# Kernel tuning notes

Hardware: AMD Instinct MI355X
Metric: run time of the kernel (lower is better)

The kernel has to match this reference:

```python
import jax, jax.numpy as jnp
import numpy as np

N_NODES = 50000
NEG_SLOPE = 0.2


def gat_conv(x, src, dst, W, att_src, att_dst, bias, concat):
    # x: [N, F_in], W: [H*D, F_in], att_*: [H, D], bias: [H*D] or [D]
    N = x.shape[0]
    H, D = att_src.shape
    h = (x @ W.T).reshape(N, H, D)                      # [N, H, D]
    a_src = jnp.einsum('nhd,hd->nh', h, att_src)        # [N, H]
    a_dst = jnp.einsum('nhd,hd->nh', h, att_dst)        # [N, H]
    e = jax.nn.leaky_relu(a_src[src] + a_dst[dst], NEG_SLOPE)  # [E, H]
    # softmax over incoming edges of each destination node
    m = jax.ops.segment_max(e, dst, num_segments=N)     # [N, H]
    ex = jnp.exp(e - m[dst])
    denom = jax.ops.segment_sum(ex, dst, num_segments=N)
    alpha = ex / denom[dst]                             # [E, H]
    msg = alpha[:, :, None] * h[src]                    # [E, H, D]
    out = jax.ops.segment_sum(msg, dst, num_segments=N) # [N, H, D]
    out = out.reshape(N, H * D) if concat else out.mean(axis=1)
    return out + bias


def setup_inputs() -> dict:
    key = jax.random.key(0)
    ks = jax.random.split(key, 10)
    nfeat, nhid, nclass, heads = 256, 128, 40, 4
    d1 = nhid // heads  # 32
    E = 800000
    x = jax.random.normal(ks[0], (N_NODES, nfeat), dtype=jnp.float32)
    edge_index = jax.random.randint(ks[1], (2, E), 0, N_NODES, dtype=jnp.int64)
    s = 0.1
    W1 = jax.random.normal(ks[2], (heads * d1, nfeat), dtype=jnp.float32) * s
    att_src1 = jax.random.normal(ks[3], (heads, d1), dtype=jnp.float32) * s
    att_dst1 = jax.random.normal(ks[4], (heads, d1), dtype=jnp.float32) * s
    b1 = jnp.zeros((heads * d1,), dtype=jnp.float32)
    W2 = jax.random.normal(ks[5], (nclass, nhid), dtype=jnp.float32) * s
    att_src2 = jax.random.normal(ks[6], (1, nclass), dtype=jnp.float32) * s
    att_dst2 = jax.random.normal(ks[7], (1, nclass), dtype=jnp.float32) * s
    b2 = jnp.zeros((nclass,), dtype=jnp.float32)
    return {"x": x, "edge_index": edge_index, "W1": W1, "att_src1": att_src1,
            "att_dst1": att_dst1, "b1": b1, "W2": W2, "att_src2": att_src2,
            "att_dst2": att_dst2, "b2": b2}


def reference(x, edge_index, W1, att_src1, att_dst1, b1, W2, att_src2, att_dst2, b2):
    # PyG GATConv adds self-loops by default
    loops = jnp.arange(N_NODES, dtype=edge_index.dtype)
    src = jnp.concatenate([edge_index[0], loops])
    dst = jnp.concatenate([edge_index[1], loops])
    h = gat_conv(x, src, dst, W1, att_src1, att_dst1, b1, concat=True)
    h = jax.nn.relu(h)
    # dropout is identity in eval mode
    out = gat_conv(h, src, dst, W2, att_src2, att_dst2, b2, concat=True)
    return out
```

## Files before the change

kernel.cpp:

```cpp
#include <hip/hip_runtime.h>
#include <hip/hip_bf16.h>
#include <cstdint>
#include <cstddef>

#define N_NODES 50000
#define NEG_SLOPE 0.2f
#define NB 196
#define BIN_CHUNK 8192
#define SLICE_MAX 14336

typedef float floatx4 __attribute__((ext_vector_type(4)));
typedef short shortx8 __attribute__((ext_vector_type(8)));

__device__ __forceinline__ unsigned short f2b(float f) {
    union { float f; unsigned u; } v; v.f = f;
    unsigned u = v.u;
    return (unsigned short)((u + 0x7FFFu + ((u >> 16) & 1u)) >> 16);
}
__device__ __forceinline__ float b2f(unsigned short b) {
    union { unsigned u; float f; } v; v.u = ((unsigned)b) << 16;
    return v.f;
}

__global__ __launch_bounds__(256) void bucket_hist_kernel(
    const int* __restrict__ ei, int E0, int E, int* __restrict__ bhist) {
    __shared__ int h[NB];
    int t = threadIdx.x;
    for (int i = t; i < NB; i += 256) h[i] = 0;
    __syncthreads();
    int base = blockIdx.x * BIN_CHUNK;
    int end = min(base + BIN_CHUNK, E);
    for (int e = base + t; e < end; e += 256) {
        int d = (e < E0) ? ei[E0 + e] : (e - E0);
        atomicAdd(&h[d >> 8], 1);
    }
    __syncthreads();
    for (int i = t; i < NB; i += 256)
        if (h[i]) atomicAdd(&bhist[i], h[i]);
}

__global__ __launch_bounds__(256) void bucket_scan_kernel(
    const int* __restrict__ bhist, int* __restrict__ bbase,
    int* __restrict__ bcursor, int* __restrict__ rowptr, int E) {
    __shared__ int buf[256];
    int t = threadIdx.x;
    int v = (t < NB) ? bhist[t] : 0;
    int x = v;
    for (int off = 1; off < 256; off <<= 1) {
        buf[t] = x; __syncthreads();
        int y = (t >= off) ? buf[t - off] : 0;
        __syncthreads();
        x += y;
    }
    if (t < NB) {
        bbase[t] = x - v;
        bcursor[t] = x - v;
    }
    if (t == NB - 1) bbase[NB] = x;
    if (t == 0) rowptr[N_NODES] = E;
}

__global__ __launch_bounds__(256) void bin_kernel(
    const int* __restrict__ ei, int E0, int E,
    int* __restrict__ bcursor, unsigned int* __restrict__ ebuf) {
    __shared__ int h[NB];
    __shared__ int gbase[NB];
    int t = threadIdx.x;
    for (int i = t; i < NB; i += 256) h[i] = 0;
    __syncthreads();
    int base = blockIdx.x * BIN_CHUNK;
    int end = min(base + BIN_CHUNK, E);
    for (int e = base + t; e < end; e += 256) {
        int d = (e < E0) ? ei[E0 + e] : (e - E0);
        atomicAdd(&h[d >> 8], 1);
    }
    __syncthreads();
    for (int i = t; i < NB; i += 256) {
        int c = h[i];
        gbase[i] = c ? atomicAdd(&bcursor[i], c) : 0;
        h[i] = 0;
    }
    __syncthreads();
    for (int e = base + t; e < end; e += 256) {
        int s, d;
        if (e < E0) { s = ei[e]; d = ei[E0 + e]; }
        else        { s = e - E0; d = e - E0; }
        int b = d >> 8;
        int off = atomicAdd(&h[b], 1);
        ebuf[gbase[b] + off] = (unsigned)s | ((unsigned)(d & 255) << 16);
    }
}

__global__ __launch_bounds__(256) void build_kernel(
    const unsigned int* __restrict__ ebuf, const int* __restrict__ bbase,
    int* __restrict__ rowptr, int* __restrict__ csr_src) {
    __shared__ int h[256];
    __shared__ int lrp[257];
    __shared__ int stag[SLICE_MAX];
    int b = blockIdx.x, t = threadIdx.x;
    int e0 = bbase[b], e1 = bbase[b + 1];
    int cnt = e1 - e0;
    int n0 = b << 8;
    h[t] = 0;
    __syncthreads();
    for (int i = t; i < cnt; i += 256)
        atomicAdd(&h[ebuf[e0 + i] >> 16], 1);
    __syncthreads();
    int v = h[t], x = v;
    __shared__ int buf[256];
    for (int off = 1; off < 256; off <<= 1) {
        buf[t] = x; __syncthreads();
        int y = (t >= off) ? buf[t - off] : 0;
        __syncthreads();
        x += y;
    }
    lrp[t] = x - v;
    if (t == 255) lrp[256] = x;
    h[t] = 0;
    __syncthreads();
    int n = n0 + t;
    if (n < N_NODES) rowptr[n] = e0 + lrp[t];
    for (int i = t; i < cnt; i += 256) {
        unsigned int v2 = ebuf[e0 + i];
        int dloc = v2 >> 16;
        int off = atomicAdd(&h[dloc], 1);
        stag[lrp[dloc] + off] = (int)(v2 & 0xFFFFu);
    }
    __syncthreads();
    for (int i = t; i < cnt; i += 256) csr_src[e0 + i] = stag[i];
}

template <int BM, int BN, int NREAL, int KK, typename InT>
__global__ __launch_bounds__(256) void gemm_bf16_kernel(
    const InT* __restrict__ A, const float* __restrict__ B,
    unsigned short* __restrict__ Cb, int M) {
    const int BK = 64, LDK = 72;
    const int NT = BN / 16;
    __shared__ unsigned short As[BM * LDK];
    __shared__ unsigned short Bs[BN * LDK];
    const int t = threadIdx.x;
    const int wave = t >> 6, lane = t & 63;
    const int lrow = lane & 15, lkg = lane >> 4;
    const int bm = blockIdx.x * BM;

    floatx4 acc[NT] = {};

    for (int k0 = 0; k0 < KK; k0 += BK) {
        __syncthreads();
        if constexpr (sizeof(InT) == 4) {
            for (int i = t; i < BM * 16; i += 256) {
                int r = i >> 4, c4 = (i & 15) << 2;
                int gr = bm + r;
                float4 v = make_float4(0.f, 0.f, 0.f, 0.f);
                if (gr < M) v = *(const float4*)&A[(size_t)gr * KK + k0 + c4];
                int o = r * LDK + c4;
                As[o] = f2b(v.x); As[o + 1] = f2b(v.y);
                As[o + 2] = f2b(v.z); As[o + 3] = f2b(v.w);
            }
        } else {
            for (int i = t; i < BM * 8; i += 256) {
                int r = i >> 3, c8 = (i & 7) << 3;
                int gr = bm + r;
                shortx8 v = {};
                if (gr < M) v = *(const shortx8*)&A[(size_t)gr * KK + k0 + c8];
                *(shortx8*)&As[r * LDK + c8] = v;
            }
        }
        for (int i = t; i < BN * 16; i += 256) {
            int r = i >> 4, c4 = (i & 15) << 2;
            float4 v = make_float4(0.f, 0.f, 0.f, 0.f);
            if (r < NREAL) v = *(const float4*)&B[(size_t)r * KK + k0 + c4];
            int o = r * LDK + c4;
            Bs[o] = f2b(v.x); Bs[o + 1] = f2b(v.y);
            Bs[o + 2] = f2b(v.z); Bs[o + 3] = f2b(v.w);
        }
        __syncthreads();

        for (int ks = 0; ks < BK; ks += 32) {
            int kc = ks + lkg * 8;
            int row = wave * 16 + lrow;
            shortx8 a = *(const shortx8*)&As[row * LDK + kc];
#pragma unroll
            for (int nt = 0; nt < NT; nt++) {
                shortx8 b = *(const shortx8*)&Bs[(nt * 16 + lrow) * LDK + kc];
                acc[nt] = __builtin_amdgcn_mfma_f32_16x16x32_bf16(a, b, acc[nt], 0, 0, 0);
            }
        }
    }
#pragma unroll
    for (int nt = 0; nt < NT; nt++)
#pragma unroll
        for (int r = 0; r < 4; r++) {
            int row = bm + wave * 16 + lkg * 4 + r;
            int col = nt * 16 + lrow;
            if (row < M && col < NREAL)
                Cb[(size_t)row * NREAL + col] = f2b(acc[nt][r]);
        }
}

__global__ void att1_kernel(const unsigned short* __restrict__ h1b,
                            const float* __restrict__ att_src,
                            const float* __restrict__ att_dst,
                            float* __restrict__ a_src, float* __restrict__ a_dst,
                            int N) {
    int i = blockIdx.x * blockDim.x + threadIdx.x;
    if (i >= N * 4) return;
    int h = i & 3;
    const ushort4* hp = (const ushort4*)(h1b + (size_t)i * 32);
    const float4* as = (const float4*)(att_src + h * 32);
    const float4* ad = (const float4*)(att_dst + h * 32);
    float ssum = 0.f, dsum = 0.f;
#pragma unroll
    for (int j = 0; j < 8; j++) {
        ushort4 hv = hp[j];
        float4 av = as[j], dv = ad[j];
        float x0 = b2f(hv.x), x1 = b2f(hv.y), x2 = b2f(hv.z), x3 = b2f(hv.w);
        ssum += x0 * av.x + x1 * av.y + x2 * av.z + x3 * av.w;
        dsum += x0 * dv.x + x1 * dv.y + x2 * dv.z + x3 * dv.w;
    }
    a_src[i] = ssum;
    a_dst[i] = dsum;
}

__global__ void att2_kernel(const unsigned short* __restrict__ h2b,
                            const float* __restrict__ att_src,
                            const float* __restrict__ att_dst,
                            float* __restrict__ a_src, float* __restrict__ a_dst,
                            int N) {
    int n = blockIdx.x * blockDim.x + threadIdx.x;
    if (n >= N) return;
    const ushort4* hp = (const ushort4*)(h2b + (size_t)n * 40);
    const float4* as = (const float4*)att_src;
    const float4* ad = (const float4*)att_dst;
    float ssum = 0.f, dsum = 0.f;
#pragma unroll
    for (int j = 0; j < 10; j++) {
        ushort4 hv = hp[j];
        float4 av = as[j], dv = ad[j];
        float x0 = b2f(hv.x), x1 = b2f(hv.y), x2 = b2f(hv.z), x3 = b2f(hv.w);
        ssum += x0 * av.x + x1 * av.y + x2 * av.z + x3 * av.w;
        dsum += x0 * dv.x + x1 * dv.y + x2 * dv.z + x3 * dv.w;
    }
    a_src[n] = ssum;
    a_dst[n] = dsum;
}

__global__ __launch_bounds__(256) void agg1_kernel(
    const unsigned short* __restrict__ h1b, const float* __restrict__ a_src,
    const float* __restrict__ a_dst, const int* __restrict__ rowptr,
    const int* __restrict__ csr_src, const float* __restrict__ b1,
    unsigned short* __restrict__ zb, int N) {
    int wave = threadIdx.x >> 6, lane = threadIdx.x & 63;
    int n = blockIdx.x * 4 + wave;
    if (n >= N) return;
    int eg = lane >> 4;
    int fpos = lane & 15;
    int hd = fpos >> 2;
    int lidx = lane >> 2;
    int lh = lane & 3;
    float adn = a_dst[n * 4 + lh];
    int beg = rowptr[n], deg = rowptr[n + 1] - beg;

    float acc[8] = {0.f, 0.f, 0.f, 0.f, 0.f, 0.f, 0.f, 0.f};
    float den = 0.f;

    int s_e = (lidx < deg) ? csr_src[beg + lidx] : 0;
    float asv = a_src[(s_e << 2) + lh];

    for (int c0 = 0; c0 < deg; c0 += 16) {
        float l = asv + adn;
        l = l > 0.f ? l : NEG_SLOPE * l;
        float w_e = (c0 + lidx < deg) ? __expf(l) : 0.f;
        int cnt = min(16, deg - c0);
        int s4[4]; float w4[4]; shortx8 v4[4];
#pragma unroll
        for (int q = 0; q < 4; q++) {
            int el = (q << 2) + eg;
            s4[q] = __shfl(s_e, el << 2);
            w4[q] = __shfl(w_e, (el << 2) + hd);
        }
#pragma unroll
        for (int q = 0; q < 4; q++) {
            if (q * 4 < cnt)
                v4[q] = *(const shortx8*)&h1b[(size_t)s4[q] * 128 + fpos * 8];
        }
        int nidx = c0 + 16 + lidx;
        int s_n = (nidx < deg) ? csr_src[beg + nidx] : 0;
        float asn = a_src[(s_n << 2) + lh];
#pragma unroll
        for (int q = 0; q < 4; q++) {
            if (q * 4 < cnt) {
                float w = w4[q];
                den += w;
#pragma unroll
                for (int j = 0; j < 8; j++)
                    acc[j] += w * b2f((unsigned short)v4[q][j]);
            }
        }
        s_e = s_n; asv = asn;
    }
#pragma unroll
    for (int j = 0; j < 8; j++) {
        acc[j] += __shfl_xor(acc[j], 16);
        acc[j] += __shfl_xor(acc[j], 32);
    }
    den += __shfl_xor(den, 16);
    den += __shfl_xor(den, 32);
    if (lane < 16) {
        float inv = 1.f / den;
        float4 bb0 = *(const float4*)&b1[fpos * 8];
        float4 bb1 = *(const float4*)&b1[fpos * 8 + 4];
        shortx8 r;
        r[0] = (short)f2b(fmaxf(acc[0] * inv + bb0.x, 0.f));
        r[1] = (short)f2b(fmaxf(acc[1] * inv + bb0.y, 0.f));
        r[2] = (short)f2b(fmaxf(acc[2] * inv + bb0.z, 0.f));
        r[3] = (short)f2b(fmaxf(acc[3] * inv + bb0.w, 0.f));
        r[4] = (short)f2b(fmaxf(acc[4] * inv + bb1.x, 0.f));
        r[5] = (short)f2b(fmaxf(acc[5] * inv + bb1.y, 0.f));
        r[6] = (short)f2b(fmaxf(acc[6] * inv + bb1.z, 0.f));
        r[7] = (short)f2b(fmaxf(acc[7] * inv + bb1.w, 0.f));
        *(shortx8*)&zb[(size_t)n * 128 + fpos * 8] = r;
    }
}

__global__ __launch_bounds__(256) void agg2_kernel(
    const unsigned short* __restrict__ h2b, const float* __restrict__ a_src,
    const float* __restrict__ a_dst, const int* __restrict__ rowptr,
    const int* __restrict__ csr_src, const float* __restrict__ b2,
    float* __restrict__ out, int N) {
    int wave = threadIdx.x >> 6, lane = threadIdx.x & 63;
    int n = blockIdx.x * 4 + wave;
    if (n >= N) return;
    int eg = (lane >= 40) ? 2 : (lane >= 20 ? 1 : 0);
    int fp = lane - eg * 20;
    bool act = fp < 20;
    float adn = a_dst[n];
    int beg = rowptr[n], deg = rowptr[n + 1] - beg;

    float2 acc = {0.f, 0.f};
    float den = 0.f;
    for (int c0 = 0; c0 < deg; c0 += 48) {
        int idx = c0 + lane;
        bool cv = (lane < 48) && (idx < deg);
        int s_e = cv ? csr_src[beg + idx] : 0;
        float l = a_src[s_e] + adn;
        l = l > 0.f ? l : NEG_SLOPE * l;
        float w_e = cv ? __expf(l) : 0.f;
        int cnt = min(48, deg - c0);
#pragma unroll
        for (int qq = 0; qq < 4; qq++) {
            if (qq * 12 < cnt) {
                int s4[4]; float w4[4]; ushort2 v4[4];
#pragma unroll
                for (int q = 0; q < 4; q++) {
                    int el = qq * 12 + q * 3 + eg;
                    s4[q] = __shfl(s_e, el);
                    w4[q] = __shfl(w_e, el);
                }
#pragma unroll
                for (int q = 0; q < 4; q++) {
                    if (act)
                        v4[q] = *(const ushort2*)&h2b[(size_t)s4[q] * 40 + fp * 2];
                }
#pragma unroll
                for (int q = 0; q < 4; q++) {
                    float w = w4[q];
                    den += w;
                    if (act) {
                        acc.x += w * b2f(v4[q].x);
                        acc.y += w * b2f(v4[q].y);
                    }
                }
            }
        }
    }
    float a1x = __shfl(acc.x, fp + 20), a2x = __shfl(acc.x, fp + 40);
    float a1y = __shfl(acc.y, fp + 20), a2y = __shfl(acc.y, fp + 40);
    float d1  = __shfl(den,  fp + 20), d2  = __shfl(den,  fp + 40);
    if (lane < 20) {
        float sx = acc.x + a1x + a2x;
        float sy = acc.y + a1y + a2y;
        float dtot = den + d1 + d2;
        float inv = 1.f / dtot;
        float2 bb = *(const float2*)&b2[fp * 2];
        float2 o;
        o.x = sx * inv + bb.x;
        o.y = sy * inv + bb.y;
        *(float2*)&out[(size_t)n * 40 + fp * 2] = o;
    }
}

extern "C" void kernel_launch(void* const* d_in, const int* in_sizes, int n_in,
                              void* d_out, int out_size, void* d_ws, size_t ws_size,
                              hipStream_t stream) {
    const float* x        = (const float*)d_in[0];
    const int*   ei       = (const int*)d_in[1];
    const float* W1       = (const float*)d_in[2];
    const float* att_src1 = (const float*)d_in[3];
    const float* att_dst1 = (const float*)d_in[4];
    const float* b1       = (const float*)d_in[5];
    const float* W2       = (const float*)d_in[6];
    const float* att_src2 = (const float*)d_in[7];
    const float* att_dst2 = (const float*)d_in[8];
    const float* b2       = (const float*)d_in[9];
    float* out = (float*)d_out;

    const int N  = N_NODES;
    const int E0 = in_sizes[1] / 2;
    const int E  = E0 + N;
    const int NBLK = (E + BIN_CHUNK - 1) / BIN_CHUNK;

    char* ws = (char*)d_ws;
    unsigned short* h1b = (unsigned short*)(ws + 0);
    unsigned short* zb  = (unsigned short*)(ws + 12800000);
    unsigned short* h2b = (unsigned short*)(ws + 25600000);
    float* a_src1 = (float*)(ws + 29600000);
    float* a_dst1 = (float*)(ws + 30400000);
    float* a_src2 = (float*)(ws + 31200000);
    float* a_dst2 = (float*)(ws + 31400000);
    int*   rowptr = (int*)(ws + 31600000);
    int*   bhist  = (int*)(ws + 31800192);
    int*   bbase  = (int*)(ws + 31801088);
    int*   bcursor= (int*)(ws + 31801984);
    unsigned int* ebuf = (unsigned int*)(ws + 31802880);
    int*   csr_src= (int*)(ws + 35202880);

    hipMemsetAsync(bhist, 0, NB * sizeof(int), stream);

    bucket_hist_kernel<<<NBLK, 256, 0, stream>>>(ei, E0, E, bhist);
    bucket_scan_kernel<<<1, 256, 0, stream>>>(bhist, bbase, bcursor, rowptr, E);
    bin_kernel<<<NBLK, 256, 0, stream>>>(ei, E0, E, bcursor, ebuf);
    build_kernel<<<NB, 256, 0, stream>>>(ebuf, bbase, rowptr, csr_src);

    gemm_bf16_kernel<64, 128, 128, 256, float>
        <<<(N + 63) / 64, 256, 0, stream>>>(x, W1, h1b, N);
    att1_kernel<<<(N * 4 + 255) / 256, 256, 0, stream>>>(h1b, att_src1, att_dst1, a_src1, a_dst1, N);
    agg1_kernel<<<(N + 3) / 4, 256, 0, stream>>>(h1b, a_src1, a_dst1, rowptr, csr_src, b1, zb, N);

    gemm_bf16_kernel<64, 48, 40, 128, unsigned short>
        <<<(N + 63) / 64, 256, 0, stream>>>(zb, W2, h2b, N);
    att2_kernel<<<(N + 255) / 256, 256, 0, stream>>>(h2b, att_src2, att_dst2, a_src2, a_dst2, N);
    agg2_kernel<<<(N + 3) / 4, 256, 0, stream>>>(h2b, a_src2, a_dst2, rowptr, csr_src, b2, out, N);
}
```

Before: 243.3 us.

## Fuse attention dot products into GEMM epilogue and reuse per-block histograms in binning

The GEMM kernels now stage the bf16 output tile in shared memory, write it out with vectorized stores, and compute the per-node a_src/a_dst attention dot products in the same epilogue. This removes the separate att1/att2 kernels and their re-read of h. The first GEMM switches to a 128-row tile with two M sub-tiles per wave. Separately, the histogram kernel saves per-block bucket counts so the binning kernel can skip its second histogram pass over the destination indices, at the cost of an extra small workspace buffer.

Result: faster. 236.9 us (-2.7%).

```diff
diff --git a/kernel.cpp b/kernel.cpp
--- a/kernel.cpp
+++ b/kernel.cpp
@@ -23,7 +23,8 @@
 }
 
 __global__ __launch_bounds__(256) void bucket_hist_kernel(
-    const int* __restrict__ ei, int E0, int E, int* __restrict__ bhist) {
+    const int* __restrict__ ei, int E0, int E, int* __restrict__ bhist,
+    int* __restrict__ bhist_blk) {
     __shared__ int h[NB];
     int t = threadIdx.x;
     for (int i = t; i < NB; i += 256) h[i] = 0;
@@ -35,8 +36,11 @@
         atomicAdd(&h[d >> 8], 1);
     }
     __syncthreads();
-    for (int i = t; i < NB; i += 256)
-        if (h[i]) atomicAdd(&bhist[i], h[i]);
+    for (int i = t; i < NB; i += 256) {
+        int c = h[i];
+        bhist_blk[blockIdx.x * NB + i] = c;
+        if (c) atomicAdd(&bhist[i], c);
+    }
 }
 
 __global__ __launch_bounds__(256) void bucket_scan_kernel(
@@ -62,25 +66,19 @@
 
 __global__ __launch_bounds__(256) void bin_kernel(
     const int* __restrict__ ei, int E0, int E,
-    int* __restrict__ bcursor, unsigned int* __restrict__ ebuf) {
+    int* __restrict__ bcursor, unsigned int* __restrict__ ebuf,
+    const int* __restrict__ bhist_blk) {
     __shared__ int h[NB];
     __shared__ int gbase[NB];
     int t = threadIdx.x;
-    for (int i = t; i < NB; i += 256) h[i] = 0;
+    for (int i = t; i < NB; i += 256) {
+        int c = bhist_blk[blockIdx.x * NB + i];
+        gbase[i] = c ? atomicAdd(&bcursor[i], c) : 0;
+        h[i] = 0;
+    }
     __syncthreads();
     int base = blockIdx.x * BIN_CHUNK;
     int end = min(base + BIN_CHUNK, E);
-    for (int e = base + t; e < end; e += 256) {
-        int d = (e < E0) ? ei[E0 + e] : (e - E0);
-        atomicAdd(&h[d >> 8], 1);
-    }
-    __syncthreads();
-    for (int i = t; i < NB; i += 256) {
-        int c = h[i];
-        gbase[i] = c ? atomicAdd(&bcursor[i], c) : 0;
-        h[i] = 0;
-    }
-    __syncthreads();
     for (int e = base + t; e < end; e += 256) {
         int s, d;
         if (e < E0) { s = ei[e]; d = ei[E0 + e]; }
@@ -130,20 +128,25 @@
     for (int i = t; i < cnt; i += 256) csr_src[e0 + i] = stag[i];
 }
 
-template <int BM, int BN, int NREAL, int KK, typename InT>
-__global__ __launch_bounds__(256) void gemm_bf16_kernel(
+template <int BM, int BN, int NREAL, int KK, int HEADS, typename InT>
+__global__ __launch_bounds__(256) void gemm_att_kernel(
     const InT* __restrict__ A, const float* __restrict__ B,
-    unsigned short* __restrict__ Cb, int M) {
+    const float* __restrict__ att_src, const float* __restrict__ att_dst,
+    unsigned short* __restrict__ Cb, float* __restrict__ a_src,
+    float* __restrict__ a_dst, int M) {
     const int BK = 64, LDK = 72;
     const int NT = BN / 16;
-    __shared__ unsigned short As[BM * LDK];
-    __shared__ unsigned short Bs[BN * LDK];
+    const int MT = BM / 64;
+    const int LDC = NREAL + 8;
+    __shared__ unsigned short smem[BM * LDK + BN * LDK];
+    unsigned short* As = smem;
+    unsigned short* Bs = smem + BM * LDK;
     const int t = threadIdx.x;
     const int wave = t >> 6, lane = t & 63;
     const int lrow = lane & 15, lkg = lane >> 4;
     const int bm = blockIdx.x * BM;
 
-    floatx4 acc[NT] = {};
+    floatx4 acc[MT][NT] = {};
 
     for (int k0 = 0; k0 < KK; k0 += BK) {
         __syncthreads();
@@ -178,71 +181,70 @@
 
         for (int ks = 0; ks < BK; ks += 32) {
             int kc = ks + lkg * 8;
-            int row = wave * 16 + lrow;
-            shortx8 a = *(const shortx8*)&As[row * LDK + kc];
-#pragma unroll
-            for (int nt = 0; nt < NT; nt++) {
-                shortx8 b = *(const shortx8*)&Bs[(nt * 16 + lrow) * LDK + kc];
-                acc[nt] = __builtin_amdgcn_mfma_f32_16x16x32_bf16(a, b, acc[nt], 0, 0, 0);
-            }
-        }
-    }
-#pragma unroll
-    for (int nt = 0; nt < NT; nt++)
-#pragma unroll
-        for (int r = 0; r < 4; r++) {
-            int row = bm + wave * 16 + lkg * 4 + r;
-            int col = nt * 16 + lrow;
-            if (row < M && col < NREAL)
-                Cb[(size_t)row * NREAL + col] = f2b(acc[nt][r]);
-        }
-}
-
-__global__ void att1_kernel(const unsigned short* __restrict__ h1b,
-                            const float* __restrict__ att_src,
-                            const float* __restrict__ att_dst,
-                            float* __restrict__ a_src, float* __restrict__ a_dst,
-                            int N) {
-    int i = blockIdx.x * blockDim.x + threadIdx.x;
-    if (i >= N * 4) return;
-    int h = i & 3;
-    const ushort4* hp = (const ushort4*)(h1b + (size_t)i * 32);
-    const float4* as = (const float4*)(att_src + h * 32);
-    const float4* ad = (const float4*)(att_dst + h * 32);
-    float ssum = 0.f, dsum = 0.f;
-#pragma unroll
-    for (int j = 0; j < 8; j++) {
-        ushort4 hv = hp[j];
-        float4 av = as[j], dv = ad[j];
-        float x0 = b2f(hv.x), x1 = b2f(hv.y), x2 = b2f(hv.z), x3 = b2f(hv.w);
-        ssum += x0 * av.x + x1 * av.y + x2 * av.z + x3 * av.w;
-        dsum += x0 * dv.x + x1 * dv.y + x2 * dv.z + x3 * dv.w;
-    }
-    a_src[i] = ssum;
-    a_dst[i] = dsum;
-}
-
-__global__ void att2_kernel(const unsigned short* __restrict__ h2b,
-                            const float* __restrict__ att_src,
-                            const float* __restrict__ att_dst,
-                            float* __restrict__ a_src, float* __restrict__ a_dst,
-                            int N) {
-    int n = blockIdx.x * blockDim.x + threadIdx.x;
-    if (n >= N) return;
-    const ushort4* hp = (const ushort4*)(h2b + (size_t)n * 40);
-    const float4* as = (const float4*)att_src;
-    const float4* ad = (const float4*)att_dst;
-    float ssum = 0.f, dsum = 0.f;
-#pragma unroll
-    for (int j = 0; j < 10; j++) {
-        ushort4 hv = hp[j];
-        float4 av = as[j], dv = ad[j];
-        float x0 = b2f(hv.x), x1 = b2f(hv.y), x2 = b2f(hv.z), x3 = b2f(hv.w);
-        ssum += x0 * av.x + x1 * av.y + x2 * av.z + x3 * av.w;
-        dsum += x0 * dv.x + x1 * dv.y + x2 * dv.z + x3 * dv.w;
-    }
-    a_src[n] = ssum;
-    a_dst[n] = dsum;
+#pragma unroll
+            for (int mt = 0; mt < MT; mt++) {
+                int row = wave * (MT * 16) + mt * 16 + lrow;
+                shortx8 a = *(const shortx8*)&As[row * LDK + kc];
+#pragma unroll
+                for (int nt = 0; nt < NT; nt++) {
+                    shortx8 b = *(const shortx8*)&Bs[(nt * 16 + lrow) * LDK + kc];
+                    acc[mt][nt] = __builtin_amdgcn_mfma_f32_16x16x32_bf16(a, b, acc[mt][nt], 0, 0, 0);
+                }
+            }
+        }
+    }
+
+    __syncthreads();
+    unsigned short* Cs = smem;
+#pragma unroll
+    for (int mt = 0; mt < MT; mt++)
+#pragma unroll
+        for (int nt = 0; nt < NT; nt++)
+#pragma unroll
+            for (int r = 0; r < 4; r++) {
+                int row = wave * (MT * 16) + mt * 16 + lkg * 4 + r;
+                int col = nt * 16 + lrow;
+                if (col < NREAL) Cs[row * LDC + col] = f2b(acc[mt][nt][r]);
+            }
+    __syncthreads();
+
+    const int NCH = NREAL / 8;
+    for (int i = t; i < BM * NCH; i += 256) {
+        int row = i / NCH, ch = i - row * NCH;
+        if (bm + row < M)
+            *(shortx8*)&Cb[(size_t)(bm + row) * NREAL + ch * 8] =
+                *(const shortx8*)&Cs[row * LDC + ch * 8];
+    }
+
+    const int D = NREAL / HEADS;
+    if (t < 2 * BM) {
+        int row = t >> 1, which = t & 1;
+        if (bm + row < M) {
+            const float* av = which ? att_dst : att_src;
+            float hs[HEADS];
+#pragma unroll
+            for (int h = 0; h < HEADS; h++) hs[h] = 0.f;
+#pragma unroll
+            for (int c = 0; c < NCH; c++) {
+                float4 p = *(const float4*)&av[c * 8];
+                float4 q = *(const float4*)&av[c * 8 + 4];
+                shortx8 cv = *(const shortx8*)&Cs[row * LDC + c * 8];
+                float s = b2f((unsigned short)cv[0]) * p.x
+                        + b2f((unsigned short)cv[1]) * p.y
+                        + b2f((unsigned short)cv[2]) * p.z
+                        + b2f((unsigned short)cv[3]) * p.w
+                        + b2f((unsigned short)cv[4]) * q.x
+                        + b2f((unsigned short)cv[5]) * q.y
+                        + b2f((unsigned short)cv[6]) * q.z
+                        + b2f((unsigned short)cv[7]) * q.w;
+                hs[(c * 8) / D] += s;
+            }
+            float* outp = which ? a_dst : a_src;
+#pragma unroll
+            for (int h = 0; h < HEADS; h++)
+                outp[(size_t)(bm + row) * HEADS + h] = hs[h];
+        }
+    }
 }
 
 __global__ __launch_bounds__(256) void agg1_kernel(
@@ -424,21 +426,22 @@
     int*   bcursor= (int*)(ws + 31801984);
     unsigned int* ebuf = (unsigned int*)(ws + 31802880);
     int*   csr_src= (int*)(ws + 35202880);
+    int*   bhist_blk = (int*)(ws + 38602880);
 
     hipMemsetAsync(bhist, 0, NB * sizeof(int), stream);
 
-    bucket_hist_kernel<<<NBLK, 256, 0, stream>>>(ei, E0, E, bhist);
+    bucket_hist_kernel<<<NBLK, 256, 0, stream>>>(ei, E0, E, bhist, bhist_blk);
     bucket_scan_kernel<<<1, 256, 0, stream>>>(bhist, bbase, bcursor, rowptr, E);
-    bin_kernel<<<NBLK, 256, 0, stream>>>(ei, E0, E, bcursor, ebuf);
+    bin_kernel<<<NBLK, 256, 0, stream>>>(ei, E0, E, bcursor, ebuf, bhist_blk);
     build_kernel<<<NB, 256, 0, stream>>>(ebuf, bbase, rowptr, csr_src);
 
-    gemm_bf16_kernel<64, 128, 128, 256, float>
-        <<<(N + 63) / 64, 256, 0, stream>>>(x, W1, h1b, N);
-    att1_kernel<<<(N * 4 + 255) / 256, 256, 0, stream>>>(h1b, att_src1, att_dst1, a_src1, a_dst1, N);
+    gemm_att_kernel<128, 128, 128, 256, 4, float>
+        <<<(N + 127) / 128, 256, 0, stream>>>(x, W1, att_src1, att_dst1,
+                                              h1b, a_src1, a_dst1, N);
     agg1_kernel<<<(N + 3) / 4, 256, 0, stream>>>(h1b, a_src1, a_dst1, rowptr, csr_src, b1, zb, N);
 
-    gemm_bf16_kernel<64, 48, 40, 128, unsigned short>
-        <<<(N + 63) / 64, 256, 0, stream>>>(zb, W2, h2b, N);
-    att2_kernel<<<(N + 255) / 256, 256, 0, stream>>>(h2b, att_src2, att_dst2, a_src2, a_dst2, N);
+    gemm_att_kernel<64, 48, 40, 128, 1, unsigned short>
+        <<<(N + 63) / 64, 256, 0, stream>>>(zb, W2, att_src2, att_dst2,
+                                            h2b, a_src2, a_dst2, N);
     agg2_kernel<<<(N + 3) / 4, 256, 0, stream>>>(h2b, a_src2, a_dst2, rowptr, csr_src, b2, out, N);
 }
```
